# Kernel optimization log

Hardware: AMD Instinct MI355X
Metric: run time of the kernel (lower is better)

## Reference

```python
import jax, jax.numpy as jnp
import numpy as np

D_MODEL = 1024
N_HEADS = 16
D_HEAD = D_MODEL // N_HEADS
SCALE = D_HEAD ** -0.5


def setup_inputs() -> dict:
    key = jax.random.key(0)
    ks = jax.random.split(key, 9)
    s = 0.02
    x = jax.random.normal(ks[0], (2, 2048, D_MODEL), dtype=jnp.float32)
    Wq = jax.random.normal(ks[1], (D_MODEL, D_MODEL), dtype=jnp.float32) * s
    Wk = jax.random.normal(ks[2], (D_MODEL, D_MODEL), dtype=jnp.float32) * s
    Wv = jax.random.normal(ks[3], (D_MODEL, D_MODEL), dtype=jnp.float32) * s
    Wo = jax.random.normal(ks[4], (D_MODEL, D_MODEL), dtype=jnp.float32) * s
    bq = jax.random.normal(ks[5], (D_MODEL,), dtype=jnp.float32) * s
    bk = jax.random.normal(ks[6], (D_MODEL,), dtype=jnp.float32) * s
    bv = jax.random.normal(ks[7], (D_MODEL,), dtype=jnp.float32) * s
    bo = jax.random.normal(ks[8], (D_MODEL,), dtype=jnp.float32) * s
    return {"x": x, "Wq": Wq, "bq": bq, "Wk": Wk, "bk": bk,
            "Wv": Wv, "bv": bv, "Wo": Wo, "bo": bo}


def reference(x, Wq, bq, Wk, bk, Wv, bv, Wo, bo):
    B, S, _ = x.shape
    # torch nn.Linear: y = x @ W.T + b
    def proj(W, b):
        h = jnp.einsum('bsd,ed->bse', x, W) + b
        return h.reshape(B, S, N_HEADS, D_HEAD).transpose(0, 2, 1, 3)  # [B,H,S,Dh]
    Q = proj(Wq, bq)
    K = proj(Wk, bk)
    V = proj(Wv, bv)
    # chunked QK^T softmax over full K == full attention (no mask, dropout=0)
    scores = jnp.einsum('bhqd,bhkd->bhqk', Q, K) * SCALE  # [B,H,S,S]
    attn = jax.nn.softmax(scores, axis=-1)
    out = jnp.einsum('bhqk,bhkd->bhqd', attn, V)
    out = out.transpose(0, 2, 1, 3).reshape(B, S, D_MODEL)
    return jnp.einsum('bsd,ed->bse', out, Wo) + bo
```

## Files before the change

kernel.cpp:

```cpp
#include <hip/hip_runtime.h>
#include <cstdint>
#include <cstddef>


typedef unsigned short u16;
typedef unsigned int u32;
typedef __bf16 bf16x8 __attribute__((ext_vector_type(8)));
typedef float f32x4 __attribute__((ext_vector_type(4)));

#define GLOAD_LDS16(gp, lp)                                                            \
  __builtin_amdgcn_global_load_lds((const __attribute__((address_space(1))) void*)(gp),\
                                   (__attribute__((address_space(3))) void*)(lp),      \
                                   16, 0, 0)

__device__ __forceinline__ u16 f2bf(float f) {
  unsigned u = __builtin_bit_cast(unsigned, f);
  u = u + 0x7fffu + ((u >> 16) & 1u);
  return (u16)(u >> 16);
}

__device__ __forceinline__ u32 pack_bf2(float a, float b) {
  u32 ua = __builtin_bit_cast(u32, a) + 0x8000u;
  u32 ub = __builtin_bit_cast(u32, b) + 0x8000u;
  return __builtin_amdgcn_perm(ub, ua, 0x07060302u);
}

#define QSCALE 0.1803368801111204f

__global__ void cvt_all(const float* __restrict__ x,
                        const float* __restrict__ wq, const float* __restrict__ wk,
                        const float* __restrict__ wv, const float* __restrict__ wo,
                        u16* __restrict__ xb, u16* __restrict__ wqb,
                        u16* __restrict__ wkb, u16* __restrict__ wvb,
                        u16* __restrict__ wob) {
  int bx = blockIdx.x;
  const float* s; u16* d; int off;
  if (bx < 2048)      { s = x;  d = xb;  off = bx; }
  else if (bx < 2560) { s = wq; d = wqb; off = bx - 2048; }
  else if (bx < 3072) { s = wk; d = wkb; off = bx - 2560; }
  else if (bx < 3584) { s = wv; d = wvb; off = bx - 3072; }
  else                { s = wo; d = wob; off = bx - 3584; }
  int i = off * 2048 + threadIdx.x * 8;
  float4 a = *(const float4*)(s + i);
  float4 b = *(const float4*)(s + i + 4);
  uint4 o;
  o.x = f2bf(a.x) | ((u32)f2bf(a.y) << 16);
  o.y = f2bf(a.z) | ((u32)f2bf(a.w) << 16);
  o.z = f2bf(b.x) | ((u32)f2bf(b.y) << 16);
  o.w = f2bf(b.z) | ((u32)f2bf(b.w) << 16);
  *(uint4*)(d + i) = o;
}

template <int MODE>
__global__ __launch_bounds__(256, 3) void gemm_mfma(
    const u16* __restrict__ A,
    const u16* __restrict__ W0, const u16* __restrict__ W1, const u16* __restrict__ W2,
    const float* __restrict__ b0, const float* __restrict__ b1, const float* __restrict__ b2,
    u16* __restrict__ o0, u16* __restrict__ o1, u16* __restrict__ o2,
    float* __restrict__ oF)
{
  __shared__ __align__(16) u16 As[128 * 64];
  __shared__ __align__(16) u16 Bs[128 * 64];

  const int tid = threadIdx.x;
  const int w = tid >> 6, l = tid & 63;
  const int lane = l & 15, quad = l >> 4;
  const int wm = w >> 1, wn = w & 1;
  const int m0 = blockIdx.y * 128;
  const int n0g = blockIdx.x * 128;

  const int src = (MODE == 0) ? (n0g >> 10) : 0;
  const u16* Wsel = (MODE == 0) ? (src == 0 ? W0 : (src == 1 ? W1 : W2)) : W0;
  const float* bsel = (MODE == 0) ? (src == 0 ? b0 : (src == 1 ? b1 : b2)) : b0;
  const int n_base = (MODE == 0) ? (n0g & 1023) : n0g;

  const int c8 = ((l & 7) ^ (l >> 3)) * 8;

  f32x4 acc[4][4] = {};

  for (int kt = 0; kt < 1024; kt += 64) {
    __syncthreads();
    const u16* Ag = A + (size_t)m0 * 1024 + kt;
    const u16* Bg = Wsel + (size_t)n_base * 1024 + kt;
    #pragma unroll
    for (int i = 0; i < 4; ++i) {
      int rr = w * 32 + i * 8;
      GLOAD_LDS16(Ag + (size_t)(rr + (l >> 3)) * 1024 + c8, As + rr * 64);
      GLOAD_LDS16(Bg + (size_t)(rr + (l >> 3)) * 1024 + c8, Bs + rr * 64);
    }
    __syncthreads();

    bf16x8 af[4][2], bf[4][2];
    #pragma unroll
    for (int mf = 0; mf < 4; ++mf)
      #pragma unroll
      for (int ks = 0; ks < 2; ++ks) {
        af[mf][ks] = *(const bf16x8*)((const char*)As +
            (wm * 64 + mf * 16 + lane) * 128 + (((ks * 4 + quad) ^ (lane & 7)) * 16));
        bf[mf][ks] = *(const bf16x8*)((const char*)Bs +
            (wn * 64 + mf * 16 + lane) * 128 + (((ks * 4 + quad) ^ (lane & 7)) * 16));
      }
    #pragma unroll
    for (int ks = 0; ks < 2; ++ks)
      #pragma unroll
      for (int mf = 0; mf < 4; ++mf)
        #pragma unroll
        for (int nf = 0; nf < 4; ++nf)
          acc[mf][nf] = __builtin_amdgcn_mfma_f32_16x16x32_bf16(
              af[mf][ks], bf[nf][ks], acc[mf][nf], 0, 0, 0);
  }

  float bb[4];
  #pragma unroll
  for (int nf = 0; nf < 4; ++nf) bb[nf] = bsel[n_base + wn * 64 + nf * 16 + lane];

  u16* osel = (MODE == 0) ? (src == 0 ? o0 : (src == 1 ? o1 : o2)) : o0;

  #pragma unroll
  for (int mf = 0; mf < 4; ++mf) {
    int mb = m0 + wm * 64 + mf * 16 + quad * 4;
    #pragma unroll
    for (int nf = 0; nf < 4; ++nf) {
      int n_l = wn * 64 + nf * 16 + lane;
      if (MODE == 0 && src == 2) {
        float v0 = acc[mf][nf][0] + bb[nf];
        float v1 = acc[mf][nf][1] + bb[nf];
        float v2 = acc[mf][nf][2] + bb[nf];
        float v3 = acc[mf][nf][3] + bb[nf];
        int bi = mb >> 11, s = mb & 2047;
        int n_in = n_base + n_l;
        int h = n_in >> 6, dh = n_in & 63;
        uint2 pk = make_uint2(pack_bf2(v0, v1), pack_bf2(v2, v3));
        *(uint2*)(o2 + (((size_t)(bi * 16 + h) * 64 + dh) * 2048 + s)) = pk;
      } else {
        #pragma unroll
        for (int r = 0; r < 4; ++r) {
          float v = acc[mf][nf][r] + bb[nf];
          int m = mb + r;
          if (MODE == 0) {
            if (src == 0) v *= QSCALE;
            int bi = m >> 11, s = m & 2047;
            int n_in = n_base + n_l;
            int h = n_in >> 6, dh = n_in & 63;
            osel[(((size_t)(bi * 16 + h) * 2048 + s) << 6) + dh] = f2bf(v);
          } else {
            oF[(size_t)m * 1024 + n0g + n_l] = v;
          }
        }
      }
    }
  }
}

__global__ __launch_bounds__(512, 4) void attn_mfma(
    const u16* __restrict__ Qg_, const u16* __restrict__ Kg_,
    const u16* __restrict__ VTg_, u16* __restrict__ Og)
{
  __shared__ __align__(16) u16 Ks[2][64 * 64];
  __shared__ __align__(16) u16 Vs[2][64 * 64];
  __shared__ __align__(16) u16 Ps[8][16 * 64];

  const int tid = threadIdx.x;
  const int w = tid >> 6, l = tid & 63;
  const int lane = l & 15, quad = l >> 4;
  const int bh = blockIdx.y;
  const int q0 = blockIdx.x * 128;

  const u16* Qg = Qg_ + ((size_t)bh * 2048 + q0) * 64;
  const u16* Kg = Kg_ + (size_t)bh * 2048 * 64;
  const u16* VTg = VTg_ + (size_t)bh * 64 * 2048;

  const int c8 = ((l & 7) ^ (l >> 3)) * 8;
  const int lrow = l >> 3;
  const int rr = w * 8;

  bf16x8 bq[2];
  #pragma unroll
  for (int ks = 0; ks < 2; ++ks)
    bq[ks] = *(const bf16x8*)(Qg +
        (size_t)(w * 16 + lane) * 64 + ks * 32 + quad * 8);

  GLOAD_LDS16(Kg + (size_t)(rr + lrow) * 64 + c8, Ks[0] + rr * 64);
  GLOAD_LDS16(VTg + (size_t)(rr + lrow) * 2048 + c8, Vs[0] + rr * 64);

  f32x4 oa[4] = {};
  float lsum = 0.f;
  u16* Pw = Ps[w];

  for (int kt = 0; kt < 32; ++kt) {
    const int buf = kt & 1;
    __syncthreads();

    if (kt < 31) {
      GLOAD_LDS16(Kg + (size_t)((kt + 1) * 64 + rr + lrow) * 64 + c8,
                  Ks[buf ^ 1] + rr * 64);
      GLOAD_LDS16(VTg + (size_t)(rr + lrow) * 2048 + (kt + 1) * 64 + c8,
                  Vs[buf ^ 1] + rr * 64);
    }

    f32x4 sa[4] = {};
    #pragma unroll
    for (int ks = 0; ks < 2; ++ks)
      #pragma unroll
      for (int kf = 0; kf < 4; ++kf) {
        bf16x8 ak = *(const bf16x8*)((const char*)Ks[buf] +
            (kf * 16 + lane) * 128 + (((ks * 4 + quad) ^ (lane & 7)) * 16));
        sa[kf] = __builtin_amdgcn_mfma_f32_16x16x32_bf16(ak, bq[ks], sa[kf], 0, 0, 0);
      }

    #pragma unroll
    for (int kf = 0; kf < 4; ++kf) {
      float p0 = __builtin_amdgcn_exp2f(sa[kf][0]);
      float p1 = __builtin_amdgcn_exp2f(sa[kf][1]);
      float p2 = __builtin_amdgcn_exp2f(sa[kf][2]);
      float p3 = __builtin_amdgcn_exp2f(sa[kf][3]);
      lsum += (p0 + p1) + (p2 + p3);
      int c = kf * 2 + (quad >> 1);
      *(uint2*)((char*)Pw + lane * 128 + ((c ^ (lane & 7)) * 16) + (quad & 1) * 8)
          = make_uint2(pack_bf2(p0, p1), pack_bf2(p2, p3));
    }

    #pragma unroll
    for (int ks = 0; ks < 2; ++ks) {
      bf16x8 ap = *(const bf16x8*)((const char*)Pw +
          lane * 128 + (((ks * 4 + quad) ^ (lane & 7)) * 16));
      #pragma unroll
      for (int df = 0; df < 4; ++df) {
        bf16x8 bv = *(const bf16x8*)((const char*)Vs[buf] +
            (df * 16 + lane) * 128 + (((ks * 4 + quad) ^ (lane & 7)) * 16));
        oa[df] = __builtin_amdgcn_mfma_f32_16x16x32_bf16(ap, bv, oa[df], 0, 0, 0);
      }
    }
  }

  lsum += __shfl_xor(lsum, 16);
  lsum += __shfl_xor(lsum, 32);

  #pragma unroll
  for (int r = 0; r < 4; ++r) {
    float inv = 1.0f / __shfl(lsum, quad * 4 + r, 16);
    int qg = q0 + w * 16 + quad * 4 + r;
    size_t base = ((size_t)(bh >> 4) * 2048 + qg) * 1024 + (bh & 15) * 64;
    #pragma unroll
    for (int df = 0; df < 4; ++df)
      Og[base + df * 16 + lane] = f2bf(oa[df][r] * inv);
  }
}

extern "C" void kernel_launch(void* const* d_in, const int* in_sizes, int n_in,
                              void* d_out, int out_size, void* d_ws, size_t ws_size,
                              hipStream_t stream)
{
  (void)in_sizes; (void)n_in; (void)out_size; (void)ws_size;
  const float* x  = (const float*)d_in[0];
  const float* Wq = (const float*)d_in[1];
  const float* bq = (const float*)d_in[2];
  const float* Wk = (const float*)d_in[3];
  const float* bk = (const float*)d_in[4];
  const float* Wv = (const float*)d_in[5];
  const float* bv = (const float*)d_in[6];
  const float* Wo = (const float*)d_in[7];
  const float* bo = (const float*)d_in[8];
  float* y = (float*)d_out;

  const size_t NM = (size_t)4096 * 1024;
  u16* xb  = (u16*)d_ws;
  u16* wqb = xb + NM;
  u16* wkb = wqb + 1024 * 1024;
  u16* wvb = wkb + 1024 * 1024;
  u16* wob = wvb + 1024 * 1024;
  u16* Qb  = wob + 1024 * 1024;
  u16* Kb  = Qb + NM;
  u16* VTb = Kb + NM;
  u16* AOb = VTb + NM;

  cvt_all<<<4096, 256, 0, stream>>>(x, Wq, Wk, Wv, Wo, xb, wqb, wkb, wvb, wob);

  gemm_mfma<0><<<dim3(24, 32), 256, 0, stream>>>(
      xb, wqb, wkb, wvb, bq, bk, bv, Qb, Kb, VTb, nullptr);

  attn_mfma<<<dim3(16, 32), 512, 0, stream>>>(Qb, Kb, VTb, AOb);

  gemm_mfma<1><<<dim3(8, 32), 256, 0, stream>>>(
      AOb, wob, nullptr, nullptr, bo, nullptr, nullptr,
      nullptr, nullptr, nullptr, y);
}
```

Baseline: 191.2 us.

## Switch attention kernel to 32x32x16 MFMA with 4 waves of 32 query rows

```diff
diff --git a/kernel.cpp b/kernel.cpp
--- a/kernel.cpp
+++ b/kernel.cpp
@@ -7,6 +7,7 @@
 typedef unsigned int u32;
 typedef __bf16 bf16x8 __attribute__((ext_vector_type(8)));
 typedef float f32x4 __attribute__((ext_vector_type(4)));
+typedef float f32x16 __attribute__((ext_vector_type(16)));
 
 #define GLOAD_LDS16(gp, lp)                                                            \
   __builtin_amdgcn_global_load_lds((const __attribute__((address_space(1))) void*)(gp),\
@@ -152,38 +153,44 @@
   }
 }
 
-__global__ __launch_bounds__(512, 4) void attn_mfma(
+__global__ __launch_bounds__(256, 2) void attn_mfma(
     const u16* __restrict__ Qg_, const u16* __restrict__ Kg_,
     const u16* __restrict__ VTg_, u16* __restrict__ Og)
 {
   __shared__ __align__(16) u16 Ks[2][64 * 64];
   __shared__ __align__(16) u16 Vs[2][64 * 64];
-  __shared__ __align__(16) u16 Ps[8][16 * 64];
+  __shared__ __align__(16) u16 Ps[4][32 * 64];
 
   const int tid = threadIdx.x;
   const int w = tid >> 6, l = tid & 63;
-  const int lane = l & 15, quad = l >> 4;
+  const int q5 = l & 31;
+  const int h  = l >> 5;
+  const int sw = q5 & 7;
   const int bh = blockIdx.y;
   const int q0 = blockIdx.x * 128;
 
-  const u16* Qg = Qg_ + ((size_t)bh * 2048 + q0) * 64;
-  const u16* Kg = Kg_ + (size_t)bh * 2048 * 64;
+  const u16* Qg  = Qg_ + ((size_t)bh * 2048 + q0 + w * 32) * 64;
+  const u16* Kg  = Kg_ + (size_t)bh * 2048 * 64;
   const u16* VTg = VTg_ + (size_t)bh * 64 * 2048;
 
   const int c8 = ((l & 7) ^ (l >> 3)) * 8;
   const int lrow = l >> 3;
-  const int rr = w * 8;
-
-  bf16x8 bq[2];
-  #pragma unroll
-  for (int ks = 0; ks < 2; ++ks)
-    bq[ks] = *(const bf16x8*)(Qg +
-        (size_t)(w * 16 + lane) * 64 + ks * 32 + quad * 8);
-
-  GLOAD_LDS16(Kg + (size_t)(rr + lrow) * 64 + c8, Ks[0] + rr * 64);
-  GLOAD_LDS16(VTg + (size_t)(rr + lrow) * 2048 + c8, Vs[0] + rr * 64);
-
-  f32x4 oa[4] = {};
+  const int rr = w * 16;
+
+  bf16x8 bq[4];
+  #pragma unroll
+  for (int s = 0; s < 4; ++s)
+    bq[s] = *(const bf16x8*)(Qg + (size_t)q5 * 64 + s * 16 + h * 8);
+
+  #pragma unroll
+  for (int i = 0; i < 2; ++i) {
+    GLOAD_LDS16(Kg + (size_t)(rr + i * 8 + lrow) * 64 + c8,
+                Ks[0] + (rr + i * 8) * 64);
+    GLOAD_LDS16(VTg + (size_t)(rr + i * 8 + lrow) * 2048 + c8,
+                Vs[0] + (rr + i * 8) * 64);
+  }
+
+  f32x16 oa[2] = {};
   float lsum = 0.f;
   u16* Pw = Ps[w];
 
@@ -192,58 +199,63 @@
     __syncthreads();
 
     if (kt < 31) {
-      GLOAD_LDS16(Kg + (size_t)((kt + 1) * 64 + rr + lrow) * 64 + c8,
-                  Ks[buf ^ 1] + rr * 64);
-      GLOAD_LDS16(VTg + (size_t)(rr + lrow) * 2048 + (kt + 1) * 64 + c8,
-                  Vs[buf ^ 1] + rr * 64);
-    }
-
-    f32x4 sa[4] = {};
-    #pragma unroll
-    for (int ks = 0; ks < 2; ++ks)
-      #pragma unroll
-      for (int kf = 0; kf < 4; ++kf) {
+      #pragma unroll
+      for (int i = 0; i < 2; ++i) {
+        GLOAD_LDS16(Kg + (size_t)((kt + 1) * 64 + rr + i * 8 + lrow) * 64 + c8,
+                    Ks[buf ^ 1] + (rr + i * 8) * 64);
+        GLOAD_LDS16(VTg + (size_t)(rr + i * 8 + lrow) * 2048 + (kt + 1) * 64 + c8,
+                    Vs[buf ^ 1] + (rr + i * 8) * 64);
+      }
+    }
+
+    f32x16 sa[2] = {};
+    #pragma unroll
+    for (int s = 0; s < 4; ++s)
+      #pragma unroll
+      for (int kt2 = 0; kt2 < 2; ++kt2) {
         bf16x8 ak = *(const bf16x8*)((const char*)Ks[buf] +
-            (kf * 16 + lane) * 128 + (((ks * 4 + quad) ^ (lane & 7)) * 16));
-        sa[kf] = __builtin_amdgcn_mfma_f32_16x16x32_bf16(ak, bq[ks], sa[kf], 0, 0, 0);
-      }
-
-    #pragma unroll
-    for (int kf = 0; kf < 4; ++kf) {
-      float p0 = __builtin_amdgcn_exp2f(sa[kf][0]);
-      float p1 = __builtin_amdgcn_exp2f(sa[kf][1]);
-      float p2 = __builtin_amdgcn_exp2f(sa[kf][2]);
-      float p3 = __builtin_amdgcn_exp2f(sa[kf][3]);
-      lsum += (p0 + p1) + (p2 + p3);
-      int c = kf * 2 + (quad >> 1);
-      *(uint2*)((char*)Pw + lane * 128 + ((c ^ (lane & 7)) * 16) + (quad & 1) * 8)
-          = make_uint2(pack_bf2(p0, p1), pack_bf2(p2, p3));
-    }
-
-    #pragma unroll
-    for (int ks = 0; ks < 2; ++ks) {
+            (kt2 * 32 + q5) * 128 + (((s * 2 + h) ^ sw) * 16));
+        sa[kt2] = __builtin_amdgcn_mfma_f32_32x32x16_bf16(ak, bq[s], sa[kt2], 0, 0, 0);
+      }
+
+    #pragma unroll
+    for (int kt2 = 0; kt2 < 2; ++kt2)
+      #pragma unroll
+      for (int g = 0; g < 4; ++g) {
+        float p0 = __builtin_amdgcn_exp2f(sa[kt2][4 * g + 0]);
+        float p1 = __builtin_amdgcn_exp2f(sa[kt2][4 * g + 1]);
+        float p2 = __builtin_amdgcn_exp2f(sa[kt2][4 * g + 2]);
+        float p3 = __builtin_amdgcn_exp2f(sa[kt2][4 * g + 3]);
+        lsum += (p0 + p1) + (p2 + p3);
+        int c = kt2 * 4 + g;
+        *(uint2*)((char*)Pw + q5 * 128 + ((c ^ sw) * 16) + 8 * h)
+            = make_uint2(pack_bf2(p0, p1), pack_bf2(p2, p3));
+      }
+
+    #pragma unroll
+    for (int ks = 0; ks < 4; ++ks) {
       bf16x8 ap = *(const bf16x8*)((const char*)Pw +
-          lane * 128 + (((ks * 4 + quad) ^ (lane & 7)) * 16));
-      #pragma unroll
-      for (int df = 0; df < 4; ++df) {
+          q5 * 128 + (((ks * 2 + h) ^ sw) * 16));
+      #pragma unroll
+      for (int dt = 0; dt < 2; ++dt) {
         bf16x8 bv = *(const bf16x8*)((const char*)Vs[buf] +
-            (df * 16 + lane) * 128 + (((ks * 4 + quad) ^ (lane & 7)) * 16));
-        oa[df] = __builtin_amdgcn_mfma_f32_16x16x32_bf16(ap, bv, oa[df], 0, 0, 0);
-      }
-    }
-  }
-
-  lsum += __shfl_xor(lsum, 16);
+            (dt * 32 + q5) * 128 + (((ks * 2 + h) ^ sw) * 16));
+        oa[dt] = __builtin_amdgcn_mfma_f32_32x32x16_bf16(ap, bv, oa[dt], 0, 0, 0);
+      }
+    }
+  }
+
   lsum += __shfl_xor(lsum, 32);
 
-  #pragma unroll
-  for (int r = 0; r < 4; ++r) {
-    float inv = 1.0f / __shfl(lsum, quad * 4 + r, 16);
-    int qg = q0 + w * 16 + quad * 4 + r;
-    size_t base = ((size_t)(bh >> 4) * 2048 + qg) * 1024 + (bh & 15) * 64;
-    #pragma unroll
-    for (int df = 0; df < 4; ++df)
-      Og[base + df * 16 + lane] = f2bf(oa[df][r] * inv);
+  const int b = bh >> 4, hh = bh & 15;
+  u16* Ob = Og + ((size_t)b * 2048 + q0 + w * 32) * 1024 + hh * 64;
+  #pragma unroll
+  for (int r = 0; r < 16; ++r) {
+    int qrow = (r & 3) + 8 * (r >> 2) + 4 * h;
+    float inv = 1.0f / __shfl(lsum, qrow);
+    #pragma unroll
+    for (int dt = 0; dt < 2; ++dt)
+      Ob[(size_t)qrow * 1024 + dt * 32 + q5] = f2bf(oa[dt][r] * inv);
   }
 }
 
@@ -279,7 +291,7 @@
   gemm_mfma<0><<<dim3(24, 32), 256, 0, stream>>>(
       xb, wqb, wkb, wvb, bq, bk, bv, Qb, Kb, VTb, nullptr);
 
-  attn_mfma<<<dim3(16, 32), 512, 0, stream>>>(Qb, Kb, VTb, AOb);
+  attn_mfma<<<dim3(16, 32), 256, 0, stream>>>(Qb, Kb, VTb, AOb);
 
   gemm_mfma<1><<<dim3(8, 32), 256, 0, stream>>>(
       AOb, wob, nullptr, nullptr, bo, nullptr, nullptr,
```

New measurement: 199.0 us. +4.1%, slower.
